# Kernel tuning notes

Measured on AMD Instinct MI355X. Metric: run time of the kernel, lower is better.

Reference implementation:

```python
import jax, jax.numpy as jnp
import numpy as np


def log_g(x):
    # log of g(x) = x + 0.5 if x >= 0 else sigmoid(x)  (minGRU paper Appendix B)
    return jnp.where(x >= 0, jnp.log(jax.nn.relu(x) + 0.5), -jax.nn.softplus(-x))


def parallel_scan_log(log_coeffs, log_values):
    # log_coeffs: [B, T, H]; log_values: [B, T+1, H]
    a_star = jnp.pad(jnp.cumsum(log_coeffs, axis=1), ((0, 0), (1, 0), (0, 0)))  # [B, T+1, H]
    log_h = a_star + jax.lax.cumlogsumexp(log_values - a_star, axis=1)
    return jnp.exp(log_h)  # [B, T+1, H]


def setup_inputs() -> dict:
    key = jax.random.key(0)
    ks = jax.random.split(key, 6)
    B, T, D, H = 4, 4096, 1024, 1024
    scale = 1.0 / np.sqrt(D)
    return {
        "x": jax.random.normal(ks[0], (B, T, D), dtype=jnp.float32),
        "h_0": jax.random.uniform(ks[1], (B, H), dtype=jnp.float32),
        "Wz": jax.random.normal(ks[2], (H, D), dtype=jnp.float32) * scale,
        "bz": jnp.zeros((H,), dtype=jnp.float32),
        "Wh": jax.random.normal(ks[3], (H, D), dtype=jnp.float32) * scale,
        "bh": jnp.zeros((H,), dtype=jnp.float32),
    }


def reference(x, h_0, Wz, bz, Wh, bh):
    T = x.shape[1]
    k = jnp.einsum("btd,hd->bth", x, Wz) + bz          # linear_z(x)
    log_z = -jax.nn.softplus(-k)                          # log sigmoid(k)
    log_coeffs = -jax.nn.softplus(k)                      # log (1 - sigmoid(k))
    log_h_0 = log_g(h_0)[:, None, :]                      # [B, 1, H]
    log_tilde_h = log_g(jnp.einsum("btd,hd->bth", x, Wh) + bh)
    log_values = jnp.concatenate([log_h_0, log_z + log_tilde_h], axis=1)  # [B, T+1, H]
    h = parallel_scan_log(log_coeffs, log_values)
    return h[:, -T:, :]
```

## Files before the change

### kernel.cpp

```cpp
#include <hip/hip_runtime.h>
#include <hip/hip_bf16.h>
#include <hip/hip_fp16.h>

#define B_ 4
#define T_ 4096
#define D_ 1024
#define H_ 1024
#define M_ (B_ * T_)

typedef __attribute__((ext_vector_type(8))) short short8;
typedef __attribute__((ext_vector_type(4))) float f32x4;

__device__ __forceinline__ unsigned short f2bf(float f) {
    unsigned int u = __float_as_uint(f);
    u += 0x7fffu + ((u >> 16) & 1u);
    return (unsigned short)(u >> 16);
}

__global__ __launch_bounds__(256) void convert_all(
    const float* __restrict__ x, const float* __restrict__ wz, const float* __restrict__ wh,
    unsigned short* __restrict__ xb, unsigned short* __restrict__ wcb)
{
    int i = blockIdx.x * 256 + threadIdx.x;
    const float* s; unsigned short* d; int soff; int doff;
    if (i < 4194304) {
        s = x; d = xb; soff = i; doff = i;
    } else if (i < 4456448) {
        int off = i - 4194304;
        int j = off >> 8; int k4 = off & 255;
        int ic = ((j >> 4) << 5) + (j & 15);
        s = wz; d = wcb; soff = off; doff = ic * 256 + k4;
    } else {
        int off = i - 4456448;
        int j = off >> 8; int k4 = off & 255;
        int ic = ((j >> 4) << 5) + 16 + (j & 15);
        s = wh; d = wcb; soff = off; doff = ic * 256 + k4;
    }
    float4 f = ((const float4*)s)[soff];
    ushort4 u;
    u.x = f2bf(f.x); u.y = f2bf(f.y); u.z = f2bf(f.z); u.w = f2bf(f.w);
    ((ushort4*)d)[doff] = u;
}

__device__ __forceinline__ void async16(const void* g, void* l) {
    __builtin_amdgcn_global_load_lds(
        (__attribute__((address_space(1))) void*)g,
        (__attribute__((address_space(3))) void*)l,
        16, 0, 0);
}

#define BARRIER() do { asm volatile("" ::: "memory"); __builtin_amdgcn_s_barrier(); asm volatile("" ::: "memory"); } while (0)
#define VMW(n)    asm volatile("s_waitcnt vmcnt(" #n ")" ::: "memory")

__global__ __launch_bounds__(512, 2) void dual_gemm_kernel(
    const unsigned short* __restrict__ xb,
    const unsigned short* __restrict__ wcb,
    const float* __restrict__ bz,
    const float* __restrict__ bh,
    __half2* __restrict__ av16,
    float2* __restrict__ chunkAV)
{
    __shared__ short8 ldsA[2 * 2 * 16 * 64];
    __shared__ short8 ldsB[2 * 2 * 16 * 64];

    const int tid  = threadIdx.x;
    const int lane = tid & 63;
    const int w    = __builtin_amdgcn_readfirstlane(tid >> 6);
    const int wr   = w >> 2;
    const int wc   = w & 3;
    const int r16  = lane & 15;
    const int q    = lane >> 4;

    const int bid = blockIdx.x;
    const int swz = (bid & 7) * 64 + (bid >> 3);
    const int nb  = swz & 7;
    const int mb  = swz >> 3;

    const int laneoff = r16 * D_ + q * 8;
    const unsigned short* gA = xb  + (size_t)(mb * 256 + 2 * w * 16) * D_ + laneoff;
    const unsigned short* gB = wcb + (size_t)(nb * 256 + 2 * w * 16) * D_ + laneoff;

#define STAGE_A(tt, kh, pp) do { \
    const unsigned short* _s = gA + (tt) * 64 + (kh) * 32; \
    short8* _d = &ldsA[(pp) * 2048 + (kh) * 1024 + 2 * w * 64]; \
    async16(_s, _d); \
    async16(_s + 16 * D_, _d + 64); } while (0)
#define STAGE_B(tt, kh, pp) do { \
    const unsigned short* _s = gB + (tt) * 64 + (kh) * 32; \
    short8* _d = &ldsB[(pp) * 2048 + (kh) * 1024 + 2 * w * 64]; \
    async16(_s, _d); \
    async16(_s + 16 * D_, _d + 64); } while (0)

    f32x4 acc[8][4] = {};

    STAGE_A(0, 0, 0); STAGE_B(0, 0, 0);
    STAGE_A(0, 1, 0); STAGE_B(0, 1, 0);
    STAGE_A(1, 0, 1); STAGE_B(1, 0, 1);
    VMW(8);
    BARRIER();

    short8 fa[4], fb[4];

#define MFMA16(MH) do { \
    _Pragma("unroll") \
    for (int m = 0; m < 4; ++m) { \
        _Pragma("unroll") \
        for (int n = 0; n < 4; ++n) \
            acc[(MH) * 4 + m][n] = __builtin_amdgcn_mfma_f32_16x16x32_bf16( \
                fa[m], fb[n], acc[(MH) * 4 + m][n], 0, 0, 0); \
    } } while (0)

    for (int g = 0; g < 16; ++g) {
        const int p  = g & 1;
        const int bA = p * 2048;
        const int oA = bA + wr * 512;
        const int oB = bA + wc * 256;

#pragma unroll
        for (int m = 0; m < 4; ++m) fa[m] = ldsA[oA + m * 64 + lane];
#pragma unroll
        for (int n = 0; n < 4; ++n) fb[n] = ldsB[oB + n * 64 + lane];
        if (g < 15) STAGE_A(g + 1, 1, p ^ 1);
        BARRIER();
        __builtin_amdgcn_s_setprio(1);
        MFMA16(0);
        __builtin_amdgcn_s_setprio(0);
        BARRIER();

#pragma unroll
        for (int m = 0; m < 4; ++m) fa[m] = ldsA[oA + (4 + m) * 64 + lane];
        if (g < 15) STAGE_B(g + 1, 1, p ^ 1);
        BARRIER();
        __builtin_amdgcn_s_setprio(1);
        MFMA16(1);
        __builtin_amdgcn_s_setprio(0);
        if (g < 15) { VMW(8); } else { VMW(0); }
        BARRIER();

#pragma unroll
        for (int m = 0; m < 4; ++m) fa[m] = ldsA[oA + 1024 + m * 64 + lane];
#pragma unroll
        for (int n = 0; n < 4; ++n) fb[n] = ldsB[oB + 1024 + n * 64 + lane];
        if (g < 14) STAGE_A(g + 2, 0, p);
        BARRIER();
        __builtin_amdgcn_s_setprio(1);
        MFMA16(0);
        __builtin_amdgcn_s_setprio(0);
        BARRIER();

#pragma unroll
        for (int m = 0; m < 4; ++m) fa[m] = ldsA[oA + 1024 + (4 + m) * 64 + lane];
        if (g < 14) STAGE_B(g + 2, 0, p);
        BARRIER();
        __builtin_amdgcn_s_setprio(1);
        MFMA16(1);
        __builtin_amdgcn_s_setprio(0);
        if (g < 14) { VMW(8); } else if (g == 14) { VMW(4); }
        BARRIER();
    }

    const int mrow0 = mb * 256 + wr * 128;
#pragma unroll
    for (int gg = 0; gg < 2; ++gg) {
        const int ncol = nb * 128 + wc * 32 + gg * 16 + r16;
        const float bzv = bz[ncol];
        const float bhv = bh[ncol];
#pragma unroll
        for (int hh = 0; hh < 2; ++hh) {
            float CA = 1.0f, CV = 0.0f;
#pragma unroll
            for (int mm = 0; mm < 4; ++mm) {
                const int mf = hh * 4 + mm;
                float LA = 1.0f, LV = 0.0f;
#pragma unroll
                for (int rr = 0; rr < 4; ++rr) {
                    float kv = acc[mf][2 * gg + 0][rr] + bzv;
                    float hv = acc[mf][2 * gg + 1][rr] + bhv;
                    float tk = __expf(-fabsf(kv));
                    float ik = 1.0f / (1.0f + tk);
                    float sig = (kv >= 0.0f) ? ik : tk * ik;
                    float ac  = (kv >= 0.0f) ? tk * ik : ik;
                    float th = __expf(-fabsf(hv));
                    float ih = 1.0f / (1.0f + th);
                    float gh = (hv >= 0.0f) ? (hv + 0.5f) : th * ih;
                    float vv = sig * gh;
                    const size_t m = (size_t)(mrow0 + mf * 16 + q * 4 + rr);
                    av16[m * H_ + ncol] = __floats2half2_rn(ac, vv);
                    LV = ac * LV + vv;
                    LA = ac * LA;
                }
#pragma unroll
                for (int mask = 16; mask <= 32; mask <<= 1) {
                    float PA = __shfl_xor(LA, mask);
                    float PV = __shfl_xor(LV, mask);
                    if (lane & mask) { LV = LA * PV + LV; LA = LA * PA; }
                    else             { LV = PA * LV + PV; LA = PA * LA; }
                }
                CV = LA * CV + LV;
                CA = LA * CA;
            }
            if (q == 0) {
                const int cglob = mb * 4 + wr * 2 + hh;
                chunkAV[(cglob & 63) * 4096 + (cglob >> 6) * 1024 + ncol] = make_float2(CA, CV);
            }
        }
    }
#undef STAGE_A
#undef STAGE_B
#undef MFMA16
}

__global__ __launch_bounds__(256) void scan_pass2(const float2* __restrict__ chunkAV,
                                                  const float* __restrict__ h0,
                                                  float* __restrict__ hstart) {
    int chan = blockIdx.x * blockDim.x + threadIdx.x;
    int n = chan & (H_ - 1);
    int b = chan >> 10;
    float x = h0[b * H_ + n];
    float h;
    if (x >= 0.0f) { h = x + 0.5f; }
    else { float t = __expf(x); h = t / (1.0f + t); }
#pragma unroll 8
    for (int c = 0; c < 64; ++c) {
        hstart[c * 4096 + chan] = h;
        float2 s = chunkAV[c * 4096 + chan];
        h = s.x * h + s.y;
    }
}

__global__ __launch_bounds__(256) void scan_pass3(const __half2* __restrict__ av16,
                                                  const float* __restrict__ hstart,
                                                  float* __restrict__ out) {
    int g = blockIdx.x * blockDim.x + threadIdx.x;
    int n = g & (H_ - 1);
    int rest = g >> 10;
    int c = rest & 63;
    int b = rest >> 6;
    float h = hstart[c * 4096 + b * 1024 + n];
    const __half2* base = av16 + ((size_t)(b * T_ + c * 64)) * H_ + n;
    float* obase = out + ((size_t)(b * T_ + c * 64)) * H_ + n;
#pragma unroll 8
    for (int t = 0; t < 64; ++t) {
        float2 p = __half22float2(base[(size_t)t * H_]);
        h = p.x * h + p.y;
        obase[(size_t)t * H_] = h;
    }
}

extern "C" void kernel_launch(void* const* d_in, const int* in_sizes, int n_in,
                              void* d_out, int out_size, void* d_ws, size_t ws_size,
                              hipStream_t stream) {
    const float* x  = (const float*)d_in[0];
    const float* h0 = (const float*)d_in[1];
    const float* Wz = (const float*)d_in[2];
    const float* bz = (const float*)d_in[3];
    const float* Wh = (const float*)d_in[4];
    const float* bh = (const float*)d_in[5];
    float* out = (float*)d_out;

    char* ws = (char*)d_ws;
    unsigned short* xb  = (unsigned short*)(ws);
    unsigned short* wcb = (unsigned short*)(ws + 33554432);
    __half2* av16       = (__half2*)(ws + 37748736);
    float2* chunkAV     = (float2*)(ws + 104857600);
    float*  hstart      = (float*)(ws + 106954752);

    convert_all<<<18432, 256, 0, stream>>>(x, Wz, Wh, xb, wcb);

    dual_gemm_kernel<<<512, 512, 0, stream>>>(xb, wcb, bz, bh, av16, chunkAV);

    scan_pass2<<<16,   256, 0, stream>>>(chunkAV, h0, hstart);
    scan_pass3<<<1024, 256, 0, stream>>>(av16, hstart, out);
}
```

Measured before the change: 273.3 us.

## Shrink dual GEMM tile to 128x128 with four waves and 2048 blocks

Measured after the change: 291.8 us. 1.07x slower.

```diff
diff --git a/kernel.cpp b/kernel.cpp
--- a/kernel.cpp
+++ b/kernel.cpp
@@ -52,7 +52,7 @@
 #define BARRIER() do { asm volatile("" ::: "memory"); __builtin_amdgcn_s_barrier(); asm volatile("" ::: "memory"); } while (0)
 #define VMW(n)    asm volatile("s_waitcnt vmcnt(" #n ")" ::: "memory")
 
-__global__ __launch_bounds__(512, 2) void dual_gemm_kernel(
+__global__ __launch_bounds__(256, 2) void dual_gemm_kernel(
     const unsigned short* __restrict__ xb,
     const unsigned short* __restrict__ wcb,
     const float* __restrict__ bz,
@@ -60,153 +60,130 @@
     __half2* __restrict__ av16,
     float2* __restrict__ chunkAV)
 {
-    __shared__ short8 ldsA[2 * 2 * 16 * 64];
-    __shared__ short8 ldsB[2 * 2 * 16 * 64];
+    __shared__ short8 ldsA[2 * 2 * 8 * 64];
+    __shared__ short8 ldsB[2 * 2 * 8 * 64];
 
     const int tid  = threadIdx.x;
     const int lane = tid & 63;
     const int w    = __builtin_amdgcn_readfirstlane(tid >> 6);
-    const int wr   = w >> 2;
-    const int wc   = w & 3;
+    const int wr   = w >> 1;
+    const int wc   = w & 1;
     const int r16  = lane & 15;
     const int q    = lane >> 4;
 
     const int bid = blockIdx.x;
-    const int swz = (bid & 7) * 64 + (bid >> 3);
-    const int nb  = swz & 7;
-    const int mb  = swz >> 3;
+    const int swz = (bid & 7) * 256 + (bid >> 3);
+    const int nb  = swz & 15;
+    const int mb  = swz >> 4;
 
     const int laneoff = r16 * D_ + q * 8;
-    const unsigned short* gA = xb  + (size_t)(mb * 256 + 2 * w * 16) * D_ + laneoff;
-    const unsigned short* gB = wcb + (size_t)(nb * 256 + 2 * w * 16) * D_ + laneoff;
-
-#define STAGE_A(tt, kh, pp) do { \
-    const unsigned short* _s = gA + (tt) * 64 + (kh) * 32; \
-    short8* _d = &ldsA[(pp) * 2048 + (kh) * 1024 + 2 * w * 64]; \
-    async16(_s, _d); \
-    async16(_s + 16 * D_, _d + 64); } while (0)
-#define STAGE_B(tt, kh, pp) do { \
-    const unsigned short* _s = gB + (tt) * 64 + (kh) * 32; \
-    short8* _d = &ldsB[(pp) * 2048 + (kh) * 1024 + 2 * w * 64]; \
-    async16(_s, _d); \
-    async16(_s + 16 * D_, _d + 64); } while (0)
-
-    f32x4 acc[8][4] = {};
-
-    STAGE_A(0, 0, 0); STAGE_B(0, 0, 0);
-    STAGE_A(0, 1, 0); STAGE_B(0, 1, 0);
-    STAGE_A(1, 0, 1); STAGE_B(1, 0, 1);
-    VMW(8);
+    const unsigned short* gA = xb  + (size_t)(mb * 128 + 2 * w * 16) * D_ + laneoff;
+    const unsigned short* gB = wcb + (size_t)(nb * 128 + 2 * w * 16) * D_ + laneoff;
+
+#define STAGE_AB(tt, kh, pp) do { \
+    const unsigned short* _sa = gA + (tt) * 64 + (kh) * 32; \
+    const unsigned short* _sb = gB + (tt) * 64 + (kh) * 32; \
+    short8* _da = &ldsA[((pp) * 2 + (kh)) * 512 + 2 * w * 64]; \
+    short8* _db = &ldsB[((pp) * 2 + (kh)) * 512 + 2 * w * 64]; \
+    async16(_sa, _da); async16(_sa + 16 * D_, _da + 64); \
+    async16(_sb, _db); async16(_sb + 16 * D_, _db + 64); } while (0)
+
+    f32x4 acc[4][4] = {};
+
+    STAGE_AB(0, 0, 0);
+    STAGE_AB(0, 1, 0);
+    VMW(4);
     BARRIER();
 
     short8 fa[4], fb[4];
 
-#define MFMA16(MH) do { \
+#define MFMA16() do { \
     _Pragma("unroll") \
     for (int m = 0; m < 4; ++m) { \
         _Pragma("unroll") \
         for (int n = 0; n < 4; ++n) \
-            acc[(MH) * 4 + m][n] = __builtin_amdgcn_mfma_f32_16x16x32_bf16( \
-                fa[m], fb[n], acc[(MH) * 4 + m][n], 0, 0, 0); \
+            acc[m][n] = __builtin_amdgcn_mfma_f32_16x16x32_bf16( \
+                fa[m], fb[n], acc[m][n], 0, 0, 0); \
     } } while (0)
 
     for (int g = 0; g < 16; ++g) {
-        const int p  = g & 1;
-        const int bA = p * 2048;
-        const int oA = bA + wr * 512;
-        const int oB = bA + wc * 256;
-
-#pragma unroll
-        for (int m = 0; m < 4; ++m) fa[m] = ldsA[oA + m * 64 + lane];
-#pragma unroll
-        for (int n = 0; n < 4; ++n) fb[n] = ldsB[oB + n * 64 + lane];
-        if (g < 15) STAGE_A(g + 1, 1, p ^ 1);
+        const int p = g & 1;
+
+        {
+            const int sA = (p * 2 + 0) * 512 + wr * 256;
+            const int sB = (p * 2 + 0) * 512 + wc * 256;
+#pragma unroll
+            for (int m = 0; m < 4; ++m) fa[m] = ldsA[sA + m * 64 + lane];
+#pragma unroll
+            for (int n = 0; n < 4; ++n) fb[n] = ldsB[sB + n * 64 + lane];
+        }
+        if (g < 15) STAGE_AB(g + 1, 0, p ^ 1);
         BARRIER();
         __builtin_amdgcn_s_setprio(1);
-        MFMA16(0);
+        MFMA16();
         __builtin_amdgcn_s_setprio(0);
-        BARRIER();
-
-#pragma unroll
-        for (int m = 0; m < 4; ++m) fa[m] = ldsA[oA + (4 + m) * 64 + lane];
-        if (g < 15) STAGE_B(g + 1, 1, p ^ 1);
+        if (g < 15) { VMW(4); } else { VMW(0); }
+        BARRIER();
+
+        {
+            const int sA = (p * 2 + 1) * 512 + wr * 256;
+            const int sB = (p * 2 + 1) * 512 + wc * 256;
+#pragma unroll
+            for (int m = 0; m < 4; ++m) fa[m] = ldsA[sA + m * 64 + lane];
+#pragma unroll
+            for (int n = 0; n < 4; ++n) fb[n] = ldsB[sB + n * 64 + lane];
+        }
+        if (g < 15) STAGE_AB(g + 1, 1, p ^ 1);
         BARRIER();
         __builtin_amdgcn_s_setprio(1);
-        MFMA16(1);
+        MFMA16();
         __builtin_amdgcn_s_setprio(0);
-        if (g < 15) { VMW(8); } else { VMW(0); }
-        BARRIER();
-
-#pragma unroll
-        for (int m = 0; m < 4; ++m) fa[m] = ldsA[oA + 1024 + m * 64 + lane];
-#pragma unroll
-        for (int n = 0; n < 4; ++n) fb[n] = ldsB[oB + 1024 + n * 64 + lane];
-        if (g < 14) STAGE_A(g + 2, 0, p);
-        BARRIER();
-        __builtin_amdgcn_s_setprio(1);
-        MFMA16(0);
-        __builtin_amdgcn_s_setprio(0);
-        BARRIER();
-
-#pragma unroll
-        for (int m = 0; m < 4; ++m) fa[m] = ldsA[oA + 1024 + (4 + m) * 64 + lane];
-        if (g < 14) STAGE_B(g + 2, 0, p);
-        BARRIER();
-        __builtin_amdgcn_s_setprio(1);
-        MFMA16(1);
-        __builtin_amdgcn_s_setprio(0);
-        if (g < 14) { VMW(8); } else if (g == 14) { VMW(4); }
-        BARRIER();
-    }
-
-    const int mrow0 = mb * 256 + wr * 128;
+        if (g < 15) VMW(4);
+        BARRIER();
+    }
+
+    const int mrow0 = mb * 128 + wr * 64;
+    const int cglob = mb * 2 + wr;
 #pragma unroll
     for (int gg = 0; gg < 2; ++gg) {
-        const int ncol = nb * 128 + wc * 32 + gg * 16 + r16;
+        const int ncol = nb * 64 + wc * 32 + gg * 16 + r16;
         const float bzv = bz[ncol];
         const float bhv = bh[ncol];
-#pragma unroll
-        for (int hh = 0; hh < 2; ++hh) {
-            float CA = 1.0f, CV = 0.0f;
-#pragma unroll
-            for (int mm = 0; mm < 4; ++mm) {
-                const int mf = hh * 4 + mm;
-                float LA = 1.0f, LV = 0.0f;
-#pragma unroll
-                for (int rr = 0; rr < 4; ++rr) {
-                    float kv = acc[mf][2 * gg + 0][rr] + bzv;
-                    float hv = acc[mf][2 * gg + 1][rr] + bhv;
-                    float tk = __expf(-fabsf(kv));
-                    float ik = 1.0f / (1.0f + tk);
-                    float sig = (kv >= 0.0f) ? ik : tk * ik;
-                    float ac  = (kv >= 0.0f) ? tk * ik : ik;
-                    float th = __expf(-fabsf(hv));
-                    float ih = 1.0f / (1.0f + th);
-                    float gh = (hv >= 0.0f) ? (hv + 0.5f) : th * ih;
-                    float vv = sig * gh;
-                    const size_t m = (size_t)(mrow0 + mf * 16 + q * 4 + rr);
-                    av16[m * H_ + ncol] = __floats2half2_rn(ac, vv);
-                    LV = ac * LV + vv;
-                    LA = ac * LA;
-                }
-#pragma unroll
-                for (int mask = 16; mask <= 32; mask <<= 1) {
-                    float PA = __shfl_xor(LA, mask);
-                    float PV = __shfl_xor(LV, mask);
-                    if (lane & mask) { LV = LA * PV + LV; LA = LA * PA; }
-                    else             { LV = PA * LV + PV; LA = PA * LA; }
-                }
-                CV = LA * CV + LV;
-                CA = LA * CA;
+        float CA = 1.0f, CV = 0.0f;
+#pragma unroll
+        for (int mf = 0; mf < 4; ++mf) {
+            float LA = 1.0f, LV = 0.0f;
+#pragma unroll
+            for (int rr = 0; rr < 4; ++rr) {
+                float kv = acc[mf][2 * gg + 0][rr] + bzv;
+                float hv = acc[mf][2 * gg + 1][rr] + bhv;
+                float tk = __expf(-fabsf(kv));
+                float ik = 1.0f / (1.0f + tk);
+                float sig = (kv >= 0.0f) ? ik : tk * ik;
+                float ac  = (kv >= 0.0f) ? tk * ik : ik;
+                float th = __expf(-fabsf(hv));
+                float ih = 1.0f / (1.0f + th);
+                float gh = (hv >= 0.0f) ? (hv + 0.5f) : th * ih;
+                float vv = sig * gh;
+                const size_t m = (size_t)(mrow0 + mf * 16 + q * 4 + rr);
+                av16[m * H_ + ncol] = __floats2half2_rn(ac, vv);
+                LV = ac * LV + vv;
+                LA = ac * LA;
             }
-            if (q == 0) {
-                const int cglob = mb * 4 + wr * 2 + hh;
-                chunkAV[(cglob & 63) * 4096 + (cglob >> 6) * 1024 + ncol] = make_float2(CA, CV);
+#pragma unroll
+            for (int mask = 16; mask <= 32; mask <<= 1) {
+                float PA = __shfl_xor(LA, mask);
+                float PV = __shfl_xor(LV, mask);
+                if (lane & mask) { LV = LA * PV + LV; LA = LA * PA; }
+                else             { LV = PA * LV + PV; LA = PA * LA; }
             }
+            CV = LA * CV + LV;
+            CA = LA * CA;
         }
-    }
-#undef STAGE_A
-#undef STAGE_B
+        if (q == 0)
+            chunkAV[(cglob & 63) * 4096 + (cglob >> 6) * 1024 + ncol] = make_float2(CA, CV);
+    }
+#undef STAGE_AB
 #undef MFMA16
 }
 
@@ -267,7 +244,7 @@
 
     convert_all<<<18432, 256, 0, stream>>>(x, Wz, Wh, xb, wcb);
 
-    dual_gemm_kernel<<<512, 512, 0, stream>>>(xb, wcb, bz, bh, av16, chunkAV);
+    dual_gemm_kernel<<<2048, 256, 0, stream>>>(xb, wcb, bz, bh, av16, chunkAV);
 
     scan_pass2<<<16,   256, 0, stream>>>(chunkAV, h0, hstart);
     scan_pass3<<<1024, 256, 0, stream>>>(av16, hstart, out);
```

## Simplify GEMM main loop to whole-tile double buffering with two barriers

Applied to the files above, without the earlier changes.

Result: no change. 272.4 us (-0.3%).

```diff
diff --git a/kernel.cpp b/kernel.cpp
--- a/kernel.cpp
+++ b/kernel.cpp
@@ -95,67 +95,62 @@
 
     STAGE_A(0, 0, 0); STAGE_B(0, 0, 0);
     STAGE_A(0, 1, 0); STAGE_B(0, 1, 0);
-    STAGE_A(1, 0, 1); STAGE_B(1, 0, 1);
-    VMW(8);
-    BARRIER();
-
-    short8 fa[4], fb[4];
-
-#define MFMA16(MH) do { \
-    _Pragma("unroll") \
-    for (int m = 0; m < 4; ++m) { \
-        _Pragma("unroll") \
-        for (int n = 0; n < 4; ++n) \
-            acc[(MH) * 4 + m][n] = __builtin_amdgcn_mfma_f32_16x16x32_bf16( \
-                fa[m], fb[n], acc[(MH) * 4 + m][n], 0, 0, 0); \
-    } } while (0)
 
     for (int g = 0; g < 16; ++g) {
         const int p  = g & 1;
-        const int bA = p * 2048;
-        const int oA = bA + wr * 512;
-        const int oB = bA + wc * 256;
-
-#pragma unroll
-        for (int m = 0; m < 4; ++m) fa[m] = ldsA[oA + m * 64 + lane];
-#pragma unroll
-        for (int n = 0; n < 4; ++n) fb[n] = ldsB[oB + n * 64 + lane];
-        if (g < 15) STAGE_A(g + 1, 1, p ^ 1);
+        const int oA = p * 2048 + wr * 512;
+        const int oB = p * 2048 + wc * 256;
+
+        if (g < 15) {
+            STAGE_A(g + 1, 0, p ^ 1);
+            STAGE_B(g + 1, 0, p ^ 1);
+            STAGE_A(g + 1, 1, p ^ 1);
+            STAGE_B(g + 1, 1, p ^ 1);
+            VMW(8);
+        } else {
+            VMW(0);
+        }
         BARRIER();
+
         __builtin_amdgcn_s_setprio(1);
-        MFMA16(0);
+        {
+            short8 fb0[4], fa0[4], fa1[4];
+#pragma unroll
+            for (int n = 0; n < 4; ++n) fb0[n] = ldsB[oB + n * 64 + lane];
+#pragma unroll
+            for (int m = 0; m < 4; ++m) fa0[m] = ldsA[oA + m * 64 + lane];
+#pragma unroll
+            for (int m = 0; m < 4; ++m) fa1[m] = ldsA[oA + (4 + m) * 64 + lane];
+#pragma unroll
+            for (int m = 0; m < 4; ++m)
+#pragma unroll
+                for (int n = 0; n < 4; ++n)
+                    acc[m][n] = __builtin_amdgcn_mfma_f32_16x16x32_bf16(fa0[m], fb0[n], acc[m][n], 0, 0, 0);
+#pragma unroll
+            for (int m = 0; m < 4; ++m)
+#pragma unroll
+                for (int n = 0; n < 4; ++n)
+                    acc[4 + m][n] = __builtin_amdgcn_mfma_f32_16x16x32_bf16(fa1[m], fb0[n], acc[4 + m][n], 0, 0, 0);
+
+            short8 fb1[4], fa2[4], fa3[4];
+#pragma unroll
+            for (int n = 0; n < 4; ++n) fb1[n] = ldsB[oB + 1024 + n * 64 + lane];
+#pragma unroll
+            for (int m = 0; m < 4; ++m) fa2[m] = ldsA[oA + 1024 + m * 64 + lane];
+#pragma unroll
+            for (int m = 0; m < 4; ++m) fa3[m] = ldsA[oA + 1024 + (4 + m) * 64 + lane];
+#pragma unroll
+            for (int m = 0; m < 4; ++m)
+#pragma unroll
+                for (int n = 0; n < 4; ++n)
+                    acc[m][n] = __builtin_amdgcn_mfma_f32_16x16x32_bf16(fa2[m], fb1[n], acc[m][n], 0, 0, 0);
+#pragma unroll
+            for (int m = 0; m < 4; ++m)
+#pragma unroll
+                for (int n = 0; n < 4; ++n)
+                    acc[4 + m][n] = __builtin_amdgcn_mfma_f32_16x16x32_bf16(fa3[m], fb1[n], acc[4 + m][n], 0, 0, 0);
+        }
         __builtin_amdgcn_s_setprio(0);
-        BARRIER();
-
-#pragma unroll
-        for (int m = 0; m < 4; ++m) fa[m] = ldsA[oA + (4 + m) * 64 + lane];
-        if (g < 15) STAGE_B(g + 1, 1, p ^ 1);
-        BARRIER();
-        __builtin_amdgcn_s_setprio(1);
-        MFMA16(1);
-        __builtin_amdgcn_s_setprio(0);
-        if (g < 15) { VMW(8); } else { VMW(0); }
-        BARRIER();
-
-#pragma unroll
-        for (int m = 0; m < 4; ++m) fa[m] = ldsA[oA + 1024 + m * 64 + lane];
-#pragma unroll
-        for (int n = 0; n < 4; ++n) fb[n] = ldsB[oB + 1024 + n * 64 + lane];
-        if (g < 14) STAGE_A(g + 2, 0, p);
-        BARRIER();
-        __builtin_amdgcn_s_setprio(1);
-        MFMA16(0);
-        __builtin_amdgcn_s_setprio(0);
-        BARRIER();
-
-#pragma unroll
-        for (int m = 0; m < 4; ++m) fa[m] = ldsA[oA + 1024 + (4 + m) * 64 + lane];
-        if (g < 14) STAGE_B(g + 2, 0, p);
-        BARRIER();
-        __builtin_amdgcn_s_setprio(1);
-        MFMA16(1);
-        __builtin_amdgcn_s_setprio(0);
-        if (g < 14) { VMW(8); } else if (g == 14) { VMW(4); }
         BARRIER();
     }
 
@@ -207,7 +202,6 @@
     }
 #undef STAGE_A
 #undef STAGE_B
-#undef MFMA16
 }
 
 __global__ __launch_bounds__(256) void scan_pass2(const float2* __restrict__ chunkAV,
```

## Pre-swizzle operands into MFMA fragment layout and load B directly to registers

Applied to the files above, without the earlier changes.

New measurement: 242.2 us. 1.13x faster.

```diff
diff --git a/kernel.cpp b/kernel.cpp
--- a/kernel.cpp
+++ b/kernel.cpp
@@ -19,27 +19,37 @@
 
 __global__ __launch_bounds__(256) void convert_all(
     const float* __restrict__ x, const float* __restrict__ wz, const float* __restrict__ wh,
-    unsigned short* __restrict__ xb, unsigned short* __restrict__ wcb)
+    unsigned short* __restrict__ xbp, unsigned short* __restrict__ wcbp)
 {
     int i = blockIdx.x * 256 + threadIdx.x;
-    const float* s; unsigned short* d; int soff; int doff;
-    if (i < 4194304) {
-        s = x; d = xb; soff = i; doff = i;
-    } else if (i < 4456448) {
-        int off = i - 4194304;
-        int j = off >> 8; int k4 = off & 255;
-        int ic = ((j >> 4) << 5) + (j & 15);
-        s = wz; d = wcb; soff = off; doff = ic * 256 + k4;
+    const float* srcrow;
+    unsigned short* dst;
+    if (i < 2097152) {
+        int l = i & 63, s = i >> 6;
+        int c = s & 31, r = s >> 5;
+        int row = r * 16 + (l & 15);
+        int k   = c * 32 + (l >> 4) * 8;
+        srcrow = x + (size_t)row * D_ + k;
+        dst = xbp + (size_t)i * 8;
     } else {
-        int off = i - 4456448;
-        int j = off >> 8; int k4 = off & 255;
-        int ic = ((j >> 4) << 5) + 16 + (j & 15);
-        s = wh; d = wcb; soff = off; doff = ic * 256 + k4;
-    }
-    float4 f = ((const float4*)s)[soff];
-    ushort4 u;
-    u.x = f2bf(f.x); u.y = f2bf(f.y); u.z = f2bf(f.z); u.w = f2bf(f.w);
-    ((ushort4*)d)[doff] = u;
+        int j = i - 2097152;
+        int l = j & 63, s = j >> 6;
+        int c = s & 31, r = s >> 5;
+        int ir = r * 16 + (l & 15);
+        int a = ir >> 5, wi = ir & 31;
+        const float* m = (wi < 16) ? wz : wh;
+        int srow = a * 16 + (wi & 15);
+        int k = c * 32 + (l >> 4) * 8;
+        srcrow = m + (size_t)srow * D_ + k;
+        dst = wcbp + (size_t)j * 8;
+    }
+    float4 f0 = ((const float4*)srcrow)[0];
+    float4 f1 = ((const float4*)srcrow)[1];
+    ushort4 u0, u1;
+    u0.x = f2bf(f0.x); u0.y = f2bf(f0.y); u0.z = f2bf(f0.z); u0.w = f2bf(f0.w);
+    u1.x = f2bf(f1.x); u1.y = f2bf(f1.y); u1.z = f2bf(f1.z); u1.w = f2bf(f1.w);
+    ((ushort4*)dst)[0] = u0;
+    ((ushort4*)dst)[1] = u1;
 }
 
 __device__ __forceinline__ void async16(const void* g, void* l) {
@@ -53,15 +63,14 @@
 #define VMW(n)    asm volatile("s_waitcnt vmcnt(" #n ")" ::: "memory")
 
 __global__ __launch_bounds__(512, 2) void dual_gemm_kernel(
-    const unsigned short* __restrict__ xb,
-    const unsigned short* __restrict__ wcb,
+    const unsigned short* __restrict__ xbp,
+    const unsigned short* __restrict__ wcbp,
     const float* __restrict__ bz,
     const float* __restrict__ bh,
     __half2* __restrict__ av16,
     float2* __restrict__ chunkAV)
 {
     __shared__ short8 ldsA[2 * 2 * 16 * 64];
-    __shared__ short8 ldsB[2 * 2 * 16 * 64];
 
     const int tid  = threadIdx.x;
     const int lane = tid & 63;
@@ -76,87 +85,83 @@
     const int nb  = swz & 7;
     const int mb  = swz >> 3;
 
-    const int laneoff = r16 * D_ + q * 8;
-    const unsigned short* gA = xb  + (size_t)(mb * 256 + 2 * w * 16) * D_ + laneoff;
-    const unsigned short* gB = wcb + (size_t)(nb * 256 + 2 * w * 16) * D_ + laneoff;
-
-#define STAGE_A(tt, kh, pp) do { \
-    const unsigned short* _s = gA + (tt) * 64 + (kh) * 32; \
-    short8* _d = &ldsA[(pp) * 2048 + (kh) * 1024 + 2 * w * 64]; \
-    async16(_s, _d); \
-    async16(_s + 16 * D_, _d + 64); } while (0)
-#define STAGE_B(tt, kh, pp) do { \
-    const unsigned short* _s = gB + (tt) * 64 + (kh) * 32; \
-    short8* _d = &ldsB[(pp) * 2048 + (kh) * 1024 + 2 * w * 64]; \
-    async16(_s, _d); \
-    async16(_s + 16 * D_, _d + 64); } while (0)
+    const unsigned short* gAp = xbp + ((size_t)mb * 16 * 32) * 512 + lane * 8;
+    const unsigned short* gBd = wcbp + ((size_t)(nb * 16 + wc * 4) * 32) * 512 + lane * 8;
+
+#define STAGE_A(tt, pp) do { \
+    _Pragma("unroll") \
+    for (int kh = 0; kh < 2; ++kh) { \
+        _Pragma("unroll") \
+        for (int d = 0; d < 2; ++d) { \
+            const unsigned short* _s = gAp + (size_t)(((2 * w + d) * 32 + (tt) * 2 + kh)) * 512; \
+            short8* _dst = &ldsA[(pp) * 2048 + kh * 1024 + (2 * w + d) * 64]; \
+            async16(_s, _dst); \
+        } } } while (0)
+
+#define LOADB(DST, tt) do { \
+    _Pragma("unroll") \
+    for (int n = 0; n < 4; ++n) { \
+        _Pragma("unroll") \
+        for (int kh = 0; kh < 2; ++kh) { \
+            DST[n][kh] = *(const short8*)(gBd + (size_t)((n * 32 + (tt) * 2 + kh)) * 512); \
+        } } } while (0)
 
     f32x4 acc[8][4] = {};
-
-    STAGE_A(0, 0, 0); STAGE_B(0, 0, 0);
-    STAGE_A(0, 1, 0); STAGE_B(0, 1, 0);
-    STAGE_A(1, 0, 1); STAGE_B(1, 0, 1);
-    VMW(8);
-    BARRIER();
-
-    short8 fa[4], fb[4];
-
-#define MFMA16(MH) do { \
-    _Pragma("unroll") \
-    for (int m = 0; m < 4; ++m) { \
-        _Pragma("unroll") \
-        for (int n = 0; n < 4; ++n) \
-            acc[(MH) * 4 + m][n] = __builtin_amdgcn_mfma_f32_16x16x32_bf16( \
-                fa[m], fb[n], acc[(MH) * 4 + m][n], 0, 0, 0); \
-    } } while (0)
-
-    for (int g = 0; g < 16; ++g) {
-        const int p  = g & 1;
-        const int bA = p * 2048;
-        const int oA = bA + wr * 512;
-        const int oB = bA + wc * 256;
-
-#pragma unroll
-        for (int m = 0; m < 4; ++m) fa[m] = ldsA[oA + m * 64 + lane];
-#pragma unroll
-        for (int n = 0; n < 4; ++n) fb[n] = ldsB[oB + n * 64 + lane];
-        if (g < 15) STAGE_A(g + 1, 1, p ^ 1);
-        BARRIER();
-        __builtin_amdgcn_s_setprio(1);
-        MFMA16(0);
-        __builtin_amdgcn_s_setprio(0);
-        BARRIER();
-
-#pragma unroll
-        for (int m = 0; m < 4; ++m) fa[m] = ldsA[oA + (4 + m) * 64 + lane];
-        if (g < 15) STAGE_B(g + 1, 1, p ^ 1);
-        BARRIER();
-        __builtin_amdgcn_s_setprio(1);
-        MFMA16(1);
-        __builtin_amdgcn_s_setprio(0);
-        if (g < 15) { VMW(8); } else { VMW(0); }
-        BARRIER();
-
-#pragma unroll
-        for (int m = 0; m < 4; ++m) fa[m] = ldsA[oA + 1024 + m * 64 + lane];
-#pragma unroll
-        for (int n = 0; n < 4; ++n) fb[n] = ldsB[oB + 1024 + n * 64 + lane];
-        if (g < 14) STAGE_A(g + 2, 0, p);
-        BARRIER();
-        __builtin_amdgcn_s_setprio(1);
-        MFMA16(0);
-        __builtin_amdgcn_s_setprio(0);
-        BARRIER();
-
-#pragma unroll
-        for (int m = 0; m < 4; ++m) fa[m] = ldsA[oA + 1024 + (4 + m) * 64 + lane];
-        if (g < 14) STAGE_B(g + 2, 0, p);
-        BARRIER();
-        __builtin_amdgcn_s_setprio(1);
-        MFMA16(1);
-        __builtin_amdgcn_s_setprio(0);
-        if (g < 14) { VMW(8); } else if (g == 14) { VMW(4); }
-        BARRIER();
+    short8 fbA[4][2], fbB[4][2];
+
+    STAGE_A(0, 0);
+    LOADB(fbA, 0);
+
+#define GROUP(g, CUR, NXT) do { \
+    const int _p = (g) & 1; \
+    if ((g) < 15) { STAGE_A((g) + 1, _p ^ 1); LOADB(NXT, (g) + 1); VMW(12); } \
+    else          { VMW(0); } \
+    BARRIER(); \
+    const int _oA = _p * 2048 + wr * 512; \
+    { \
+        short8 fa0[4], fa1[4]; \
+        _Pragma("unroll") \
+        for (int m = 0; m < 4; ++m) fa0[m] = ldsA[_oA + m * 64 + lane]; \
+        _Pragma("unroll") \
+        for (int m = 0; m < 4; ++m) fa1[m] = ldsA[_oA + (4 + m) * 64 + lane]; \
+        __builtin_amdgcn_s_setprio(1); \
+        _Pragma("unroll") \
+        for (int m = 0; m < 4; ++m) \
+            _Pragma("unroll") \
+            for (int n = 0; n < 4; ++n) \
+                acc[m][n] = __builtin_amdgcn_mfma_f32_16x16x32_bf16(fa0[m], CUR[n][0], acc[m][n], 0, 0, 0); \
+        _Pragma("unroll") \
+        for (int m = 0; m < 4; ++m) \
+            _Pragma("unroll") \
+            for (int n = 0; n < 4; ++n) \
+                acc[4 + m][n] = __builtin_amdgcn_mfma_f32_16x16x32_bf16(fa1[m], CUR[n][0], acc[4 + m][n], 0, 0, 0); \
+        __builtin_amdgcn_s_setprio(0); \
+    } \
+    { \
+        short8 fa2[4], fa3[4]; \
+        _Pragma("unroll") \
+        for (int m = 0; m < 4; ++m) fa2[m] = ldsA[_oA + 1024 + m * 64 + lane]; \
+        _Pragma("unroll") \
+        for (int m = 0; m < 4; ++m) fa3[m] = ldsA[_oA + 1024 + (4 + m) * 64 + lane]; \
+        __builtin_amdgcn_s_setprio(1); \
+        _Pragma("unroll") \
+        for (int m = 0; m < 4; ++m) \
+            _Pragma("unroll") \
+            for (int n = 0; n < 4; ++n) \
+                acc[m][n] = __builtin_amdgcn_mfma_f32_16x16x32_bf16(fa2[m], CUR[n][1], acc[m][n], 0, 0, 0); \
+        _Pragma("unroll") \
+        for (int m = 0; m < 4; ++m) \
+            _Pragma("unroll") \
+            for (int n = 0; n < 4; ++n) \
+                acc[4 + m][n] = __builtin_amdgcn_mfma_f32_16x16x32_bf16(fa3[m], CUR[n][1], acc[4 + m][n], 0, 0, 0); \
+        __builtin_amdgcn_s_setprio(0); \
+    } \
+    BARRIER(); \
+} while (0)
+
+    for (int it = 0; it < 8; ++it) {
+        GROUP(2 * it,     fbA, fbB);
+        GROUP(2 * it + 1, fbB, fbA);
     }
 
     const int mrow0 = mb * 256 + wr * 128;
@@ -206,8 +211,8 @@
         }
     }
 #undef STAGE_A
-#undef STAGE_B
-#undef MFMA16
+#undef LOADB
+#undef GROUP
 }
 
 __global__ __launch_bounds__(256) void scan_pass2(const float2* __restrict__ chunkAV,
@@ -259,15 +264,15 @@
     float* out = (float*)d_out;
 
     char* ws = (char*)d_ws;
-    unsigned short* xb  = (unsigned short*)(ws);
-    unsigned short* wcb = (unsigned short*)(ws + 33554432);
-    __half2* av16       = (__half2*)(ws + 37748736);
-    float2* chunkAV     = (float2*)(ws + 104857600);
-    float*  hstart      = (float*)(ws + 106954752);
-
-    convert_all<<<18432, 256, 0, stream>>>(x, Wz, Wh, xb, wcb);
-
-    dual_gemm_kernel<<<512, 512, 0, stream>>>(xb, wcb, bz, bh, av16, chunkAV);
+    unsigned short* xbp  = (unsigned short*)(ws);
+    unsigned short* wcbp = (unsigned short*)(ws + 33554432);
+    __half2* av16        = (__half2*)(ws + 37748736);
+    float2* chunkAV      = (float2*)(ws + 104857600);
+    float*  hstart       = (float*)(ws + 106954752);
+
+    convert_all<<<9216, 256, 0, stream>>>(x, Wz, Wh, xbp, wcbp);
+
+    dual_gemm_kernel<<<512, 512, 0, stream>>>(xbp, wcbp, bz, bh, av16, chunkAV);
 
     scan_pass2<<<16,   256, 0, stream>>>(chunkAV, h0, hstart);
     scan_pass3<<<1024, 256, 0, stream>>>(av16, hstart, out);
```
